# Kernel tuning notes

Hardware: AMD Instinct MI355X
Metric: run time of the kernel (lower is better)

Reference implementation:

```python
import jax, jax.numpy as jnp
import numpy as np

EMBED_DIM = 1024
NUM_HEADS = 16
HEAD_DIM = EMBED_DIM // NUM_HEADS
QUANTUM_HEADS = 2
BATCH = 2
SEQ = 2048


def setup_inputs() -> dict:
    key = jax.random.key(0)
    ks = jax.random.split(key, 12)
    s = 1.0 / np.sqrt(EMBED_DIM)
    d = {
        "x": jax.random.normal(ks[0], (BATCH, SEQ, EMBED_DIM), jnp.float32),
        "Wq": jax.random.normal(ks[1], (EMBED_DIM, EMBED_DIM), jnp.float32) * s,
        "bq": jax.random.normal(ks[2], (EMBED_DIM,), jnp.float32) * s,
        "Wk": jax.random.normal(ks[3], (EMBED_DIM, EMBED_DIM), jnp.float32) * s,
        "bk": jax.random.normal(ks[4], (EMBED_DIM,), jnp.float32) * s,
        "Wv": jax.random.normal(ks[5], (EMBED_DIM, EMBED_DIM), jnp.float32) * s,
        "bv": jax.random.normal(ks[6], (EMBED_DIM,), jnp.float32) * s,
        "Wo": jax.random.normal(ks[7], (EMBED_DIM, EMBED_DIM), jnp.float32) * s,
        "bo": jax.random.normal(ks[8], (EMBED_DIM,), jnp.float32) * s,
        # surrogate params for the per-head quantum expectation layers
        "qw": jax.random.normal(ks[9], (QUANTUM_HEADS,), jnp.float32),
        "qb": jax.random.normal(ks[10], (QUANTUM_HEADS,), jnp.float32) * 0.1,
    }
    return d


def reference(x, Wq, bq, Wk, bk, Wv, bv, Wo, bo, qw, qb):
    B, S, E = x.shape
    H, D, QH = NUM_HEADS, HEAD_DIM, QUANTUM_HEADS

    def proj(W, b):  # nn.Linear: x @ W.T + b, then split heads -> (B,H,S,D)
        y = jnp.einsum("bse,fe->bsf", x, W) + b
        return y.reshape(B, S, H, D).transpose(0, 2, 1, 3)

    q = proj(Wq, bq)
    k = proj(Wk, bk)
    v = proj(Wv, bv)

    scores = jnp.einsum("bhsd,bhtd->bhst", q, k) / jnp.sqrt(jnp.float32(D))
    attn = jax.nn.softmax(scores, axis=-1)  # (B,H,S,S)

    # quantum-head post-softmax rescaling: per (batch, quantum head) scalar
    agg = attn[:, :QH].mean(axis=(2, 3))            # (B,QH)
    refined = jnp.cos(qw[None, :] * agg + qb[None, :])  # surrogate expectation in [-1,1]
    scale = jnp.concatenate(
        [refined, jnp.ones((B, H - QH), dtype=attn.dtype)], axis=1
    )  # (B,H)
    attn = attn * scale[:, :, None, None]

    out = jnp.einsum("bhst,bhtd->bhsd", attn, v)
    out = out.transpose(0, 2, 1, 3).reshape(B, S, E)
    out = jnp.einsum("bse,fe->bsf", out, Wo) + bo
    return out
```

## Files before the change

### kernel.cpp

```cpp
#include <hip/hip_runtime.h>
#include <hip/hip_bf16.h>

#define B_ 2
#define S_ 2048
#define E_ 1024
#define H_ 16
#define D_ 64

typedef __attribute__((ext_vector_type(8))) short short8;
typedef __attribute__((ext_vector_type(4))) float f32x4;
typedef __attribute__((ext_vector_type(16))) float f32x16;
typedef __attribute__((ext_vector_type(4))) unsigned short u16x4;

#define AS1 __attribute__((address_space(1)))
#define AS3 __attribute__((address_space(3)))

static __device__ __forceinline__ unsigned short f2bf(float f) {
  unsigned int u = __builtin_bit_cast(unsigned int, f);
  return (unsigned short)((u + 0x7fffu + ((u >> 16) & 1u)) >> 16);
}
static __device__ __forceinline__ unsigned short f2bf_f(float f) {
  unsigned int u = __builtin_bit_cast(unsigned int, f);
  return (unsigned short)((u + 0x8000u) >> 16);
}
static __device__ __forceinline__ void gload_lds16(const void* g, void* l) {
  __builtin_amdgcn_global_load_lds((const AS1 unsigned int*)g, (AS3 unsigned int*)l, 16, 0, 0);
}

__global__ __launch_bounds__(256) void cvt_all(const float* __restrict__ x,
                                               const float* __restrict__ w0,
                                               const float* __restrict__ w1,
                                               const float* __restrict__ w2,
                                               const float* __restrict__ w3,
                                               unsigned short* __restrict__ xb,
                                               unsigned short* __restrict__ wcat) {
  const int y = blockIdx.y;
  const float* src;
  unsigned short* dst;
  if (y < 4) {
    src = (y == 0) ? w0 : (y == 1) ? w1 : (y == 2) ? w2 : w3;
    dst = wcat + (size_t)y * (E_ * E_);
  } else {
    src = x + (size_t)(y - 4) * (E_ * E_);
    dst = xb + (size_t)(y - 4) * (E_ * E_);
  }
  int i = blockIdx.x * 1024 + threadIdx.x * 4;
  f32x4 v = *(const f32x4*)(src + i);
  u16x4 o;
  o.x = f2bf(v.x); o.y = f2bf(v.y); o.z = f2bf(v.z); o.w = f2bf(v.w);
  *(u16x4*)(dst + i) = o;
}

__global__ __launch_bounds__(256) void gemm_qkv3(const unsigned short* __restrict__ A,
                                                 const unsigned short* __restrict__ W,
                                                 const float* __restrict__ bq,
                                                 const float* __restrict__ bk,
                                                 const float* __restrict__ bv,
                                                 unsigned short* __restrict__ Qo,
                                                 unsigned short* __restrict__ Ko,
                                                 unsigned short* __restrict__ VT) {
  __shared__ unsigned short lA[128 * 32];
  __shared__ unsigned short lB[128 * 32];
  const int K = E_;
  const int tid  = threadIdx.x;
  const int lane = tid & 63;
  const int w    = tid >> 6;
  const int wm   = (w >> 1) * 64, wn = (w & 1) * 64;
  const int li   = lane & 15, quad = lane >> 4;
  const int m0   = blockIdx.x * 128, n0 = blockIdx.y * 128;

  f32x4 acc[4][4];
#pragma unroll
  for (int i = 0; i < 4; ++i)
#pragma unroll
    for (int j = 0; j < 4; ++j) { f32x4 z = {0.f, 0.f, 0.f, 0.f}; acc[i][j] = z; }

  const int r0 = tid >> 2, kc0 = (tid & 3) * 8;
  const unsigned short* a0 = A + (size_t)(m0 + r0) * K + kc0;
  const unsigned short* a1 = A + (size_t)(m0 + r0 + 64) * K + kc0;
  const unsigned short* b0 = W + (size_t)(n0 + r0) * K + kc0;
  const unsigned short* b1 = W + (size_t)(n0 + r0 + 64) * K + kc0;

  for (int k0 = 0; k0 < K; k0 += 32) {
    __syncthreads();
    gload_lds16(a0 + k0, &lA[tid * 8]);
    gload_lds16(a1 + k0, &lA[(tid + 256) * 8]);
    gload_lds16(b0 + k0, &lB[tid * 8]);
    gload_lds16(b1 + k0, &lB[(tid + 256) * 8]);
    __syncthreads();
    short8 af[4], bf[4];
#pragma unroll
    for (int i = 0; i < 4; ++i) af[i] = *(const short8*)&lA[(wm + i * 16 + li) * 32 + quad * 8];
#pragma unroll
    for (int j = 0; j < 4; ++j) bf[j] = *(const short8*)&lB[(wn + j * 16 + li) * 32 + quad * 8];
#pragma unroll
    for (int i = 0; i < 4; ++i)
#pragma unroll
      for (int j = 0; j < 4; ++j)
        acc[i][j] = __builtin_amdgcn_mfma_f32_16x16x32_bf16(af[i], bf[j], acc[i][j], 0, 0, 0);
  }

  const int third = blockIdx.y >> 3;
  if (third < 2) {
    unsigned short* C = (third == 0) ? Qo : Ko;
    const float* bias = (third == 0) ? bq : bk;
    const float sc = (third == 0) ? 0.125f : 1.0f;
#pragma unroll
    for (int j = 0; j < 4; ++j) {
      int colf = (n0 & 1023) + wn + j * 16 + li;
      float bvv = bias[colf];
#pragma unroll
      for (int i = 0; i < 4; ++i)
#pragma unroll
        for (int r = 0; r < 4; ++r) {
          int row = m0 + wm + i * 16 + quad * 4 + r;
          C[(size_t)row * E_ + colf] = f2bf_f((acc[i][j][r] + bvv) * sc);
        }
    }
  } else {
#pragma unroll
    for (int j = 0; j < 4; ++j) {
      int colf = (n0 & 1023) + wn + j * 16 + li;
      int h2 = colf >> 6, d2 = colf & 63;
      float bvv = bv[colf];
#pragma unroll
      for (int i = 0; i < 4; ++i) {
        int srow = m0 + wm + i * 16 + quad * 4;
        int bb = srow >> 11, s2 = srow & 2047;
        u16x4 o;
        o.x = f2bf_f(acc[i][j][0] + bvv);
        o.y = f2bf_f(acc[i][j][1] + bvv);
        o.z = f2bf_f(acc[i][j][2] + bvv);
        o.w = f2bf_f(acc[i][j][3] + bvv);
        *(u16x4*)&VT[(((size_t)bb * 16 + h2) * 64 + d2) * 2048 + s2] = o;
      }
    }
  }
}

__global__ __launch_bounds__(256) void gemm_out64(const unsigned short* __restrict__ A,
                                                  const unsigned short* __restrict__ W,
                                                  const float* __restrict__ bias,
                                                  float* __restrict__ C) {
  __shared__ unsigned short lA[64 * 32];
  __shared__ unsigned short lB[128 * 32];
  const int N = E_, K = E_;
  const int tid  = threadIdx.x;
  const int lane = tid & 63;
  const int w    = tid >> 6;
  const int m0   = blockIdx.x * 64, n0 = blockIdx.y * 128;
  const int mi   = (w >> 1) * 32, ni = (w & 1) * 64;
  const int li   = lane & 15, quad = lane >> 4, koff = quad * 8;

  f32x4 acc[2][4];
#pragma unroll
  for (int i = 0; i < 2; ++i)
#pragma unroll
    for (int j = 0; j < 4; ++j) { f32x4 z = {0.f, 0.f, 0.f, 0.f}; acc[i][j] = z; }

  const int arow = tid >> 2, ak = (tid & 3) * 8;
  const int b2 = tid + 256;

  for (int k0 = 0; k0 < K; k0 += 32) {
    __syncthreads();
    gload_lds16(A + (size_t)(m0 + arow) * K + k0 + ak, &lA[tid * 8]);
    gload_lds16(W + (size_t)(n0 + arow) * K + k0 + ak, &lB[tid * 8]);
    gload_lds16(W + (size_t)(n0 + (b2 >> 2)) * K + k0 + (b2 & 3) * 8, &lB[b2 * 8]);
    __syncthreads();
    short8 a0 = *(const short8*)&lA[(mi      + li) * 32 + koff];
    short8 a1 = *(const short8*)&lA[(mi + 16 + li) * 32 + koff];
#pragma unroll
    for (int nt = 0; nt < 4; ++nt) {
      short8 bb = *(const short8*)&lB[(ni + nt * 16 + li) * 32 + koff];
      acc[0][nt] = __builtin_amdgcn_mfma_f32_16x16x32_bf16(a0, bb, acc[0][nt], 0, 0, 0);
      acc[1][nt] = __builtin_amdgcn_mfma_f32_16x16x32_bf16(a1, bb, acc[1][nt], 0, 0, 0);
    }
  }

#pragma unroll
  for (int mt = 0; mt < 2; ++mt)
#pragma unroll
    for (int nt = 0; nt < 4; ++nt) {
      int col = n0 + ni + nt * 16 + li;
      float bvv = bias[col];
#pragma unroll
      for (int r = 0; r < 4; ++r) {
        int row = m0 + mi + mt * 16 + quad * 4 + r;
        C[(size_t)row * N + col] = acc[mt][nt][r] + bvv;
      }
    }
}

__global__ __launch_bounds__(512, 4) void attn_kernel(const unsigned short* __restrict__ Q,
                                                      const unsigned short* __restrict__ Kp,
                                                      const unsigned short* __restrict__ VT,
                                                      const float* __restrict__ qw,
                                                      const float* __restrict__ qb,
                                                      unsigned short* __restrict__ O) {
  __shared__ __align__(16) char smem[49152];
  unsigned short* Qs = (unsigned short*)smem;
  unsigned short* Ks = (unsigned short*)(smem + 16384);
  unsigned short* Vs = (unsigned short*)(smem + 32768);
  float* Rbuf = (float*)(smem + 16384);
  float* Lbuf = (float*)smem;

  const int tid  = threadIdx.x;
  const int lane = tid & 63;
  const int c    = lane & 31, hi = lane >> 5;
  const int wv   = tid >> 6, wq = wv & 3, wt = wv >> 2;
  const int s0 = blockIdx.x * 128, h = blockIdx.y, b = blockIdx.z;
  const int cm7 = c & 7;

  {
    int p = tid, row = p >> 3, kc = (p & 7) ^ (row & 7);
    gload_lds16(Q + (size_t)(b * S_ + s0 + row) * E_ + h * 64 + kc * 8, &Qs[p * 8]);
    p = tid + 512; row = p >> 3; kc = (p & 7) ^ (row & 7);
    gload_lds16(Q + (size_t)(b * S_ + s0 + row) * E_ + h * 64 + kc * 8, &Qs[p * 8]);
  }
  const int kr1 = tid >> 3, kr2 = (tid + 512) >> 3;
  const unsigned short* kg1 = Kp + (size_t)(b * S_ + kr1) * E_ + h * 64 + (((tid & 7) ^ (kr1 & 7)) * 8);
  const unsigned short* kg2 = Kp + (size_t)(b * S_ + kr2) * E_ + h * 64 + ((((tid + 512) & 7) ^ (kr2 & 7)) * 8);
  const int vr1 = tid >> 4, vr2 = (tid + 512) >> 4;
  const unsigned short* vg1 = VT + ((size_t)((b * H_ + h) * 64 + vr1)) * S_ + (((tid & 15) ^ (vr1 & 7)) * 8);
  const unsigned short* vg2 = VT + ((size_t)((b * H_ + h) * 64 + vr2)) * S_ + ((((tid + 512) & 15) ^ (vr2 & 7)) * 8);

  __syncthreads();

  short8 qf[4];
#pragma unroll
  for (int kk = 0; kk < 4; ++kk)
    qf[kk] = *(const short8*)&Qs[(wq * 32 + c) * 64 + (((2 * kk + hi) ^ cm7) << 3)];

  f32x16 ot[2];
#pragma unroll
  for (int d = 0; d < 2; ++d)
#pragma unroll
    for (int i = 0; i < 16; ++i) ot[d][i] = 0.f;
  float lacc = 0.f;

  for (int tt = 0; tt < S_ / 128; ++tt) {
    if (tt) __syncthreads();
    gload_lds16(kg1, &Ks[tid * 8]);
    gload_lds16(kg2, &Ks[(tid + 512) * 8]);
    gload_lds16(vg1, &Vs[tid * 8]);
    gload_lds16(vg2, &Vs[(tid + 512) * 8]);
    kg1 += (size_t)128 * E_; kg2 += (size_t)128 * E_;
    vg1 += 128; vg2 += 128;
    __syncthreads();

    f32x16 st[2];
#pragma unroll
    for (int d = 0; d < 2; ++d)
#pragma unroll
      for (int i = 0; i < 16; ++i) st[d][i] = 0.f;
#pragma unroll
    for (int tau = 0; tau < 2; ++tau) {
      const int trow = 64 * wt + 32 * tau + c;
#pragma unroll
      for (int kk = 0; kk < 4; ++kk) {
        short8 kf = *(const short8*)&Ks[trow * 64 + (((2 * kk + hi) ^ cm7) << 3)];
        st[tau] = __builtin_amdgcn_mfma_f32_32x32x16_bf16(kf, qf[kk], st[tau], 0, 0, 0);
      }
    }

    unsigned int pk[2][8];
#pragma unroll
    for (int tau = 0; tau < 2; ++tau)
#pragma unroll
      for (int m = 0; m < 4; ++m)
#pragma unroll
        for (int u = 0; u < 2; ++u) {
          float p0 = __expf(st[tau][4 * m + 2 * u]);
          float p1 = __expf(st[tau][4 * m + 2 * u + 1]);
          lacc += p0 + p1;
          pk[tau][2 * m + u] = (unsigned int)f2bf_f(p0) | ((unsigned int)f2bf_f(p1) << 16);
        }

#pragma unroll
    for (int pp = 0; pp < 2; ++pp)
#pragma unroll
      for (int tau = 0; tau < 2; ++tau) {
        unsigned int q0a = pk[tau][4 * pp + 0], q0b = pk[tau][4 * pp + 1];
        unsigned int q1a = pk[tau][4 * pp + 2], q1b = pk[tau][4 * pp + 3];
        unsigned int sa = hi ? q0a : q1a, sb = hi ? q0b : q1b;
        unsigned int ra = (unsigned int)__shfl_xor((int)sa, 32, 64);
        unsigned int rb = (unsigned int)__shfl_xor((int)sb, 32, 64);
        unsigned int oa = hi ? q1a : q0a, ob = hi ? q1b : q0b;
        unsigned int l0 = hi ? ra : oa, l1 = hi ? rb : ob;
        unsigned int h0 = hi ? oa : ra, h1 = hi ? ob : rb;
        union { unsigned int u[4]; short8 s; } bf;
        bf.u[0] = l0; bf.u[1] = l1; bf.u[2] = h0; bf.u[3] = h1;
        const int j = 2 * tau + pp;
#pragma unroll
        for (int dd = 0; dd < 2; ++dd) {
          short8 vf = *(const short8*)&Vs[(32 * dd + c) * 128 + (((8 * wt + 2 * j + hi) ^ cm7) << 3)];
          ot[dd] = __builtin_amdgcn_mfma_f32_32x32x16_bf16(vf, bf.s, ot[dd], 0, 0, 0);
        }
      }
  }

  float l2 = lacc + __shfl_xor(lacc, 32, 64);

  __syncthreads();
  if (wt == 1) {
#pragma unroll
    for (int dd = 0; dd < 2; ++dd)
#pragma unroll
      for (int i = 0; i < 16; ++i) Rbuf[(wq * 64 + lane) * 32 + dd * 16 + i] = ot[dd][i];
    Lbuf[wq * 64 + lane] = l2;
  }
  __syncthreads();
  if (wt == 0) {
    float lt = l2 + Lbuf[wq * 64 + lane];
    float scale = 1.0f;
    if (h < 2) scale = cosf(qw[h] * (1.0f / (float)S_) + qb[h]);
    float inv = scale / lt;
    const int q = s0 + wq * 32 + c;
    unsigned short* obase = O + (size_t)(b * S_ + q) * E_ + h * 64;
#pragma unroll
    for (int dd = 0; dd < 2; ++dd)
#pragma unroll
      for (int m = 0; m < 4; ++m) {
        u16x4 o;
#pragma unroll
        for (int r = 0; r < 4; ++r) {
          float v = (ot[dd][4 * m + r] + Rbuf[(wq * 64 + lane) * 32 + dd * 16 + 4 * m + r]) * inv;
          ((unsigned short*)&o)[r] = f2bf_f(v);
        }
        *(u16x4*)(obase + 32 * dd + 8 * m + 4 * hi) = o;
      }
  }
}

extern "C" void kernel_launch(void* const* d_in, const int* in_sizes, int n_in,
                              void* d_out, int out_size, void* d_ws, size_t ws_size,
                              hipStream_t stream) {
  const float* x  = (const float*)d_in[0];
  const float* Wq = (const float*)d_in[1];
  const float* bq = (const float*)d_in[2];
  const float* Wk = (const float*)d_in[3];
  const float* bk = (const float*)d_in[4];
  const float* Wv = (const float*)d_in[5];
  const float* bv = (const float*)d_in[6];
  const float* Wo = (const float*)d_in[7];
  const float* bo = (const float*)d_in[8];
  const float* qw = (const float*)d_in[9];
  const float* qb = (const float*)d_in[10];
  float* out = (float*)d_out;

  char* ws = (char*)d_ws;
  const size_t MB = 1u << 20;
  unsigned short* xb   = (unsigned short*)(ws + 0 * MB);
  unsigned short* Wcat = (unsigned short*)(ws + 8 * MB);
  unsigned short* Qb   = (unsigned short*)(ws + 16 * MB);
  unsigned short* Kb   = (unsigned short*)(ws + 24 * MB);
  unsigned short* VTb  = (unsigned short*)(ws + 32 * MB);
  unsigned short* Ob   = (unsigned short*)(ws + 40 * MB);
  unsigned short* Wob  = Wcat + (size_t)3 * E_ * E_;

  cvt_all<<<dim3(1024, 8), 256, 0, stream>>>(x, Wq, Wk, Wv, Wo, xb, Wcat);

  gemm_qkv3<<<dim3(32, 24), 256, 0, stream>>>(xb, Wcat, bq, bk, bv, Qb, Kb, VTb);

  attn_kernel<<<dim3(S_ / 128, H_, B_), 512, 0, stream>>>(Qb, Kb, VTb, qw, qb, Ob);

  gemm_out64<<<dim3(64, 8), 256, 0, stream>>>(Ob, Wob, bo, out);
}
```

Measured before the change: 212.8 us.

## Double-buffer attention K/V tiles, widen GEMM K-step with swizzled LDS, stage V transpose

The attention kernel now double-buffers its K/V tiles in LDS. It prefetches the next tile while computing the current one and keeps only one barrier per iteration. Both GEMMs move from a K-step of 32 to 64 with an XOR-swizzled LDS layout, which halves the barrier count and reduces bank conflicts. The V-transpose epilogue is staged through LDS so global stores become coalesced 16-byte rows, and the reduction buffer is padded to stride 33. The cost is that attention LDS grows to 80KB, which may cut resident blocks per CU below the launch-bound target.

```diff
diff --git a/kernel.cpp b/kernel.cpp
--- a/kernel.cpp
+++ b/kernel.cpp
@@ -59,14 +59,16 @@
                                                  unsigned short* __restrict__ Qo,
                                                  unsigned short* __restrict__ Ko,
                                                  unsigned short* __restrict__ VT) {
-  __shared__ unsigned short lA[128 * 32];
-  __shared__ unsigned short lB[128 * 32];
+  __shared__ __align__(16) unsigned short sm[128 * 64 * 2];
+  unsigned short* lA = sm;
+  unsigned short* lB = sm + 128 * 64;
   const int K = E_;
   const int tid  = threadIdx.x;
   const int lane = tid & 63;
   const int w    = tid >> 6;
   const int wm   = (w >> 1) * 64, wn = (w & 1) * 64;
   const int li   = lane & 15, quad = lane >> 4;
+  const int e7   = li & 7;
   const int m0   = blockIdx.x * 128, n0 = blockIdx.y * 128;
 
   f32x4 acc[4][4];
@@ -75,29 +77,37 @@
 #pragma unroll
     for (int j = 0; j < 4; ++j) { f32x4 z = {0.f, 0.f, 0.f, 0.f}; acc[i][j] = z; }
 
-  const int r0 = tid >> 2, kc0 = (tid & 3) * 8;
-  const unsigned short* a0 = A + (size_t)(m0 + r0) * K + kc0;
-  const unsigned short* a1 = A + (size_t)(m0 + r0 + 64) * K + kc0;
-  const unsigned short* b0 = W + (size_t)(n0 + r0) * K + kc0;
-  const unsigned short* b1 = W + (size_t)(n0 + r0 + 64) * K + kc0;
-
-  for (int k0 = 0; k0 < K; k0 += 32) {
-    __syncthreads();
-    gload_lds16(a0 + k0, &lA[tid * 8]);
-    gload_lds16(a1 + k0, &lA[(tid + 256) * 8]);
-    gload_lds16(b0 + k0, &lB[tid * 8]);
-    gload_lds16(b1 + k0, &lB[(tid + 256) * 8]);
-    __syncthreads();
-    short8 af[4], bf[4];
-#pragma unroll
-    for (int i = 0; i < 4; ++i) af[i] = *(const short8*)&lA[(wm + i * 16 + li) * 32 + quad * 8];
-#pragma unroll
-    for (int j = 0; j < 4; ++j) bf[j] = *(const short8*)&lB[(wn + j * 16 + li) * 32 + quad * 8];
-#pragma unroll
-    for (int i = 0; i < 4; ++i)
+  const unsigned short* pA[4];
+  const unsigned short* pB[4];
+#pragma unroll
+  for (int q = 0; q < 4; ++q) {
+    int p = tid + 256 * q, row = p >> 3, kc = (p & 7) ^ (row & 7);
+    pA[q] = A + (size_t)(m0 + row) * K + kc * 8;
+    pB[q] = W + (size_t)(n0 + row) * K + kc * 8;
+  }
+
+  for (int k0 = 0; k0 < K; k0 += 64) {
+    __syncthreads();
+#pragma unroll
+    for (int q = 0; q < 4; ++q) gload_lds16(pA[q] + k0, &lA[(tid + 256 * q) * 8]);
+#pragma unroll
+    for (int q = 0; q < 4; ++q) gload_lds16(pB[q] + k0, &lB[(tid + 256 * q) * 8]);
+    __syncthreads();
+#pragma unroll
+    for (int ks = 0; ks < 2; ++ks) {
+      short8 af[4], bf[4];
+#pragma unroll
+      for (int i = 0; i < 4; ++i)
+        af[i] = *(const short8*)&lA[(wm + i * 16 + li) * 64 + (((ks * 4 + quad) ^ e7) << 3)];
 #pragma unroll
       for (int j = 0; j < 4; ++j)
-        acc[i][j] = __builtin_amdgcn_mfma_f32_16x16x32_bf16(af[i], bf[j], acc[i][j], 0, 0, 0);
+        bf[j] = *(const short8*)&lB[(wn + j * 16 + li) * 64 + (((ks * 4 + quad) ^ e7) << 3)];
+#pragma unroll
+      for (int i = 0; i < 4; ++i)
+#pragma unroll
+        for (int j = 0; j < 4; ++j)
+          acc[i][j] = __builtin_amdgcn_mfma_f32_16x16x32_bf16(af[i], bf[j], acc[i][j], 0, 0, 0);
+    }
   }
 
   const int third = blockIdx.y >> 3;
@@ -118,22 +128,36 @@
         }
     }
   } else {
+    const int base = (blockIdx.y & 7) * 128;
+    __syncthreads();
 #pragma unroll
     for (int j = 0; j < 4; ++j) {
-      int colf = (n0 & 1023) + wn + j * 16 + li;
-      int h2 = colf >> 6, d2 = colf & 63;
-      float bvv = bv[colf];
+      int col = wn + j * 16 + li;
+      float bvv = bv[base + col];
+      int cm15 = col & 15;
 #pragma unroll
       for (int i = 0; i < 4; ++i) {
-        int srow = m0 + wm + i * 16 + quad * 4;
-        int bb = srow >> 11, s2 = srow & 2047;
+        int s = wm + i * 16 + quad * 4;
+        int off = col * 128 + (((s >> 3) ^ cm15) << 3) + (s & 7);
         u16x4 o;
         o.x = f2bf_f(acc[i][j][0] + bvv);
         o.y = f2bf_f(acc[i][j][1] + bvv);
         o.z = f2bf_f(acc[i][j][2] + bvv);
         o.w = f2bf_f(acc[i][j][3] + bvv);
-        *(u16x4*)&VT[(((size_t)bb * 16 + h2) * 64 + d2) * 2048 + s2] = o;
-      }
+        *(u16x4*)&sm[off] = o;
+      }
+    }
+    __syncthreads();
+    int col = tid >> 1, half = tid & 1;
+    int colf = base + col;
+    int h2 = colf >> 6, d2 = colf & 63;
+    int bb = m0 >> 11, s2 = m0 & 2047;
+    unsigned short* dst = VT + (((size_t)bb * 16 + h2) * 64 + d2) * 2048 + s2 + half * 64;
+    int cm15 = col & 15;
+#pragma unroll
+    for (int u = 0; u < 8; ++u) {
+      int sc2 = half * 8 + u;
+      *(short8*)(dst + u * 8) = *(const short8*)&sm[col * 128 + ((sc2 ^ cm15) << 3)];
     }
   }
 }
@@ -142,15 +166,16 @@
                                                   const unsigned short* __restrict__ W,
                                                   const float* __restrict__ bias,
                                                   float* __restrict__ C) {
-  __shared__ unsigned short lA[64 * 32];
-  __shared__ unsigned short lB[128 * 32];
+  __shared__ __align__(16) unsigned short lA[64 * 64];
+  __shared__ __align__(16) unsigned short lB[128 * 64];
   const int N = E_, K = E_;
   const int tid  = threadIdx.x;
   const int lane = tid & 63;
   const int w    = tid >> 6;
   const int m0   = blockIdx.x * 64, n0 = blockIdx.y * 128;
   const int mi   = (w >> 1) * 32, ni = (w & 1) * 64;
-  const int li   = lane & 15, quad = lane >> 4, koff = quad * 8;
+  const int li   = lane & 15, quad = lane >> 4;
+  const int e7   = li & 7;
 
   f32x4 acc[2][4];
 #pragma unroll
@@ -158,22 +183,36 @@
 #pragma unroll
     for (int j = 0; j < 4; ++j) { f32x4 z = {0.f, 0.f, 0.f, 0.f}; acc[i][j] = z; }
 
-  const int arow = tid >> 2, ak = (tid & 3) * 8;
-  const int b2 = tid + 256;
-
-  for (int k0 = 0; k0 < K; k0 += 32) {
-    __syncthreads();
-    gload_lds16(A + (size_t)(m0 + arow) * K + k0 + ak, &lA[tid * 8]);
-    gload_lds16(W + (size_t)(n0 + arow) * K + k0 + ak, &lB[tid * 8]);
-    gload_lds16(W + (size_t)(n0 + (b2 >> 2)) * K + k0 + (b2 & 3) * 8, &lB[b2 * 8]);
-    __syncthreads();
-    short8 a0 = *(const short8*)&lA[(mi      + li) * 32 + koff];
-    short8 a1 = *(const short8*)&lA[(mi + 16 + li) * 32 + koff];
-#pragma unroll
-    for (int nt = 0; nt < 4; ++nt) {
-      short8 bb = *(const short8*)&lB[(ni + nt * 16 + li) * 32 + koff];
-      acc[0][nt] = __builtin_amdgcn_mfma_f32_16x16x32_bf16(a0, bb, acc[0][nt], 0, 0, 0);
-      acc[1][nt] = __builtin_amdgcn_mfma_f32_16x16x32_bf16(a1, bb, acc[1][nt], 0, 0, 0);
+  const unsigned short* pA[2];
+  const unsigned short* pB[4];
+#pragma unroll
+  for (int q = 0; q < 2; ++q) {
+    int p = tid + 256 * q, row = p >> 3, kc = (p & 7) ^ (row & 7);
+    pA[q] = A + (size_t)(m0 + row) * K + kc * 8;
+  }
+#pragma unroll
+  for (int q = 0; q < 4; ++q) {
+    int p = tid + 256 * q, row = p >> 3, kc = (p & 7) ^ (row & 7);
+    pB[q] = W + (size_t)(n0 + row) * K + kc * 8;
+  }
+
+  for (int k0 = 0; k0 < K; k0 += 64) {
+    __syncthreads();
+#pragma unroll
+    for (int q = 0; q < 2; ++q) gload_lds16(pA[q] + k0, &lA[(tid + 256 * q) * 8]);
+#pragma unroll
+    for (int q = 0; q < 4; ++q) gload_lds16(pB[q] + k0, &lB[(tid + 256 * q) * 8]);
+    __syncthreads();
+#pragma unroll
+    for (int ks = 0; ks < 2; ++ks) {
+      short8 a0 = *(const short8*)&lA[(mi      + li) * 64 + (((ks * 4 + quad) ^ e7) << 3)];
+      short8 a1 = *(const short8*)&lA[(mi + 16 + li) * 64 + (((ks * 4 + quad) ^ e7) << 3)];
+#pragma unroll
+      for (int nt = 0; nt < 4; ++nt) {
+        short8 bb = *(const short8*)&lB[(ni + nt * 16 + li) * 64 + (((ks * 4 + quad) ^ e7) << 3)];
+        acc[0][nt] = __builtin_amdgcn_mfma_f32_16x16x32_bf16(a0, bb, acc[0][nt], 0, 0, 0);
+        acc[1][nt] = __builtin_amdgcn_mfma_f32_16x16x32_bf16(a1, bb, acc[1][nt], 0, 0, 0);
+      }
     }
   }
 
@@ -197,10 +236,12 @@
                                                       const float* __restrict__ qw,
                                                       const float* __restrict__ qb,
                                                       unsigned short* __restrict__ O) {
-  __shared__ __align__(16) char smem[49152];
+  __shared__ __align__(16) char smem[81920];
   unsigned short* Qs = (unsigned short*)smem;
-  unsigned short* Ks = (unsigned short*)(smem + 16384);
-  unsigned short* Vs = (unsigned short*)(smem + 32768);
+  unsigned short* KsB0 = (unsigned short*)(smem + 16384);
+  unsigned short* VsB0 = (unsigned short*)(smem + 32768);
+  unsigned short* KsB1 = (unsigned short*)(smem + 49152);
+  unsigned short* VsB1 = (unsigned short*)(smem + 65536);
   float* Rbuf = (float*)(smem + 16384);
   float* Lbuf = (float*)smem;
 
@@ -224,6 +265,12 @@
   const unsigned short* vg1 = VT + ((size_t)((b * H_ + h) * 64 + vr1)) * S_ + (((tid & 15) ^ (vr1 & 7)) * 8);
   const unsigned short* vg2 = VT + ((size_t)((b * H_ + h) * 64 + vr2)) * S_ + ((((tid + 512) & 15) ^ (vr2 & 7)) * 8);
 
+  gload_lds16(kg1, &KsB0[tid * 8]);
+  gload_lds16(kg2, &KsB0[(tid + 512) * 8]);
+  gload_lds16(vg1, &VsB0[tid * 8]);
+  gload_lds16(vg2, &VsB0[(tid + 512) * 8]);
+  kg1 += (size_t)128 * E_; kg2 += (size_t)128 * E_;
+  vg1 += 128; vg2 += 128;
   __syncthreads();
 
   short8 qf[4];
@@ -238,15 +285,20 @@
     for (int i = 0; i < 16; ++i) ot[d][i] = 0.f;
   float lacc = 0.f;
 
+#pragma unroll 2
   for (int tt = 0; tt < S_ / 128; ++tt) {
-    if (tt) __syncthreads();
-    gload_lds16(kg1, &Ks[tid * 8]);
-    gload_lds16(kg2, &Ks[(tid + 512) * 8]);
-    gload_lds16(vg1, &Vs[tid * 8]);
-    gload_lds16(vg2, &Vs[(tid + 512) * 8]);
-    kg1 += (size_t)128 * E_; kg2 += (size_t)128 * E_;
-    vg1 += 128; vg2 += 128;
-    __syncthreads();
+    if (tt < S_ / 128 - 1) {
+      unsigned short* Kn = ((tt + 1) & 1) ? KsB1 : KsB0;
+      unsigned short* Vn = ((tt + 1) & 1) ? VsB1 : VsB0;
+      gload_lds16(kg1, &Kn[tid * 8]);
+      gload_lds16(kg2, &Kn[(tid + 512) * 8]);
+      gload_lds16(vg1, &Vn[tid * 8]);
+      gload_lds16(vg2, &Vn[(tid + 512) * 8]);
+      kg1 += (size_t)128 * E_; kg2 += (size_t)128 * E_;
+      vg1 += 128; vg2 += 128;
+    }
+    const unsigned short* Ks = (tt & 1) ? KsB1 : KsB0;
+    const unsigned short* Vs = (tt & 1) ? VsB1 : VsB0;
 
     f32x16 st[2];
 #pragma unroll
@@ -297,16 +349,16 @@
           ot[dd] = __builtin_amdgcn_mfma_f32_32x32x16_bf16(vf, bf.s, ot[dd], 0, 0, 0);
         }
       }
+    __syncthreads();
   }
 
   float l2 = lacc + __shfl_xor(lacc, 32, 64);
 
-  __syncthreads();
   if (wt == 1) {
 #pragma unroll
     for (int dd = 0; dd < 2; ++dd)
 #pragma unroll
-      for (int i = 0; i < 16; ++i) Rbuf[(wq * 64 + lane) * 32 + dd * 16 + i] = ot[dd][i];
+      for (int i = 0; i < 16; ++i) Rbuf[(wq * 64 + lane) * 33 + dd * 16 + i] = ot[dd][i];
     Lbuf[wq * 64 + lane] = l2;
   }
   __syncthreads();
@@ -324,7 +376,7 @@
         u16x4 o;
 #pragma unroll
         for (int r = 0; r < 4; ++r) {
-          float v = (ot[dd][4 * m + r] + Rbuf[(wq * 64 + lane) * 32 + dd * 16 + 4 * m + r]) * inv;
+          float v = (ot[dd][4 * m + r] + Rbuf[(wq * 64 + lane) * 33 + dd * 16 + 4 * m + r]) * inv;
           ((unsigned short*)&o)[r] = f2bf_f(v);
         }
         *(u16x4*)(obase + 32 * dd + 8 * m + 4 * hi) = o;
```

New measurement: 201.6 us. 1.06x faster.
